# Optimization experiments

Measured on AMD Instinct MI355X. Metric: run time of the kernel, lower is better.

The kernel has to match this reference:

```python
import jax
import jax.numpy as jnp
from jax import lax
import numpy as np

B, C, H, W = 16, 96, 112, 112
HIDDEN = 4 * C
LN_EPS = 1e-6  # ConvNeXt LayerNorm eps


def setup_inputs() -> dict:
    key = jax.random.key(0)
    ks = jax.random.split(key, 8)
    x = jax.random.normal(ks[0], (B, C, H, W), dtype=jnp.float32)
    # depthwise 7x7 kernel, HWIO with feature_group_count=C -> (7,7,1,C)
    dw_w = jax.random.normal(ks[1], (7, 7, 1, C), dtype=jnp.float32) * 0.02
    dw_b = jnp.zeros((C,), dtype=jnp.float32)
    gamma = jnp.ones((C,), dtype=jnp.float32)
    beta = jnp.zeros((C,), dtype=jnp.float32)
    w1 = jax.random.normal(ks[2], (C, HIDDEN), dtype=jnp.float32) * 0.02
    b1 = jnp.zeros((HIDDEN,), dtype=jnp.float32)
    w2 = jax.random.normal(ks[3], (HIDDEN, C), dtype=jnp.float32) * 0.02
    b2 = jnp.zeros((C,), dtype=jnp.float32)
    scale = jnp.full((C,), 1e-6, dtype=jnp.float32)  # block_scale init 1e-6
    return {"x": x, "dw_w": dw_w, "dw_b": dw_b, "gamma": gamma, "beta": beta,
            "w1": w1, "b1": b1, "w2": w2, "b2": b2, "scale": scale}


def reference(x, dw_w, dw_b, gamma, beta, w1, b1, w2, b2, scale):
    # depthwise 7x7, stride 1, padding 3 (SAME), groups = C
    y = lax.conv_general_dilated(
        x, dw_w, window_strides=(1, 1), padding="SAME",
        dimension_numbers=("NCHW", "HWIO", "NCHW"),
        feature_group_count=C,
    ) + dw_b[None, :, None, None]
    # BCHW -> BHWC
    y = jnp.transpose(y, (0, 2, 3, 1))
    # LayerNorm over channel dim
    mu = jnp.mean(y, axis=-1, keepdims=True)
    var = jnp.var(y, axis=-1, keepdims=True)
    y = (y - mu) * lax.rsqrt(var + LN_EPS) * gamma + beta
    # pointwise MLP with exact GELU (torch nn.GELU default)
    h = jax.nn.gelu(jnp.einsum("bhwc,cd->bhwd", y, w1) + b1, approximate=False)
    y = jnp.einsum("bhwd,dc->bhwc", h, w2) + b2
    # BHWC -> BCHW, scale, residual (eval mode: stochastic depth = identity)
    y = jnp.transpose(y, (0, 3, 1, 2))
    return scale[None, :, None, None] * y + x
```

## Files before the change

### kernel.cpp

```cpp
#include <hip/hip_runtime.h>
#include <hip/hip_bf16.h>

#define BATCH 16
#define CCH 96
#define HH 112
#define WW 112
#define HID 384
#define NPIX (BATCH * HH * WW)
#define HW (HH * WW)

#define PXB 128
#define ZROWD 50
#define HSLICE 6144
#define RING_SLOTS 6
#define ZR_BYTES (PXB * ZROWD * 4)
#define B1_OFF (RING_SLOTS * HSLICE)
#define SMEM_TOTAL (B1_OFF + 1536)

typedef __attribute__((ext_vector_type(8))) short bf16x8;
typedef __attribute__((ext_vector_type(4))) float f32x4;
typedef __attribute__((ext_vector_type(4))) unsigned int uint4v;

typedef const __attribute__((address_space(1))) void gvoid_t;
typedef __attribute__((address_space(3))) void svoid_t;

__device__ __forceinline__ short f2bf(float v) {
    __hip_bfloat16 h = __float2bfloat16(v);
    return __builtin_bit_cast(short, h);
}
__device__ __forceinline__ float bf2f(short s) {
    unsigned int u = ((unsigned int)(unsigned short)s) << 16;
    return __builtin_bit_cast(float, u);
}
__device__ __forceinline__ float gelu_fast(float v) {
    float e = __expf(-1.702f * v);
    return v * __builtin_amdgcn_rcpf(1.0f + e);
}

__global__ __launch_bounds__(256) void pack_w(const float* __restrict__ w1,
                                              const float* __restrict__ w2,
                                              const float* __restrict__ gamma,
                                              const float* __restrict__ scale,
                                              short* __restrict__ wp) {
    int o = blockIdx.x * 256 + threadIdx.x;
    if (o >= 12 * 12 * 64 * 8) return;
    const int j   = o & 7;
    const int l   = (o >> 3) & 63;
    const int g   = o >> 9;
    const int f   = g % 12;
    const int kk2 = g / 12;
    float v;
    if (f < 6) {
        const int kk = f >> 1, mh = f & 1;
        const int c  = kk * 32 + (l >> 4) * 8 + j;
        const int d  = (2 * kk2 + mh) * 16 + (l & 15);
        v = gamma[c] * w1[c * HID + d];
    } else {
        const int nt2 = f - 6;
        const int dd  = kk2 * 32 + ((j >> 2) << 4) + ((l >> 4) << 2) + (j & 3);
        const int n   = nt2 * 16 + (l & 15);
        v = w2[dd * CCH + n] * scale[n];
    }
    wp[o] = f2bf(v);
}

__global__ __launch_bounds__(256) void pack_bias(const float* __restrict__ w1,
                                                 const float* __restrict__ b1,
                                                 const float* __restrict__ beta,
                                                 const float* __restrict__ b2,
                                                 const float* __restrict__ scale,
                                                 float* __restrict__ b1p,
                                                 float* __restrict__ b2p) {
    int t = blockIdx.x * 256 + threadIdx.x;
    if (t < HID) {
        float s = b1[t];
        for (int c = 0; c < CCH; ++c) s += beta[c] * w1[c * HID + t];
        b1p[t] = s;
    } else if (t < HID + CCH) {
        int c = t - HID;
        b2p[c] = scale[c] * b2[c];
    }
}

__global__ __launch_bounds__(256) void conv_kernel(
    const float* __restrict__ x, const float* __restrict__ dww,
    const float* __restrict__ dwb, short* __restrict__ y)
{
    __shared__ float xs[34][128];

    const int t = threadIdx.x;
    const int p = blockIdx.x;
    int o = (p & 7) * 768 + (p >> 3);
    const int ht = o & 3;  o >>= 2;
    const int c  = o % CCH;
    const int b  = o / CCH;
    const int h0 = ht * 28;
    const float* xc = x + (size_t)(b * CCH + c) * HW;

    float4 vbuf[5];
    #pragma unroll
    for (int k = 0; k < 5; ++k) {
        const int idx = t + 256 * k;
        const int r  = idx >> 5;
        const int j  = idx & 31;
        const int gh = h0 - 3 + r;
        float4 v = make_float4(0.f, 0.f, 0.f, 0.f);
        if (idx < 1088 && (unsigned)gh < HH && j >= 1 && j <= 28)
            v = *reinterpret_cast<const float4*>(xc + gh * WW + 4 * j - 4);
        vbuf[k] = v;
    }
    #pragma unroll
    for (int k = 0; k < 5; ++k) {
        const int idx = t + 256 * k;
        if (idx < 1088)
            *reinterpret_cast<float4*>(&xs[0][0] + (idx >> 5) * 128 + (idx & 31) * 4) = vbuf[k];
    }
    __syncthreads();

    const int col = t & 127;
    const int rg  = t >> 7;
    if (col < WW) {
        const int r0 = rg * 14;
        const float bias = dwb[c];
        float acc[14];
        #pragma unroll
        for (int r = 0; r < 14; ++r) acc[r] = bias;
        #pragma unroll
        for (int kw = 0; kw < 7; ++kw) {
            float cv[20];
            #pragma unroll
            for (int i = 0; i < 20; ++i) cv[i] = xs[r0 + i][col + kw + 1];
            #pragma unroll
            for (int kh = 0; kh < 7; ++kh) {
                const float wt = dww[(kh * 7 + kw) * CCH + c];
                #pragma unroll
                for (int r = 0; r < 14; ++r) acc[r] += cv[r + kh] * wt;
            }
        }
        short* yc = y + (size_t)(b * CCH + c) * HW + (h0 + r0) * WW + col;
        #pragma unroll
        for (int r = 0; r < 14; ++r) yc[r * WW] = f2bf(acc[r]);
    }
}

__global__ __launch_bounds__(256, 4) void mlp_kernel(
    const short* __restrict__ ybuf, const char* __restrict__ wp,
    const float* __restrict__ b1p, const float* __restrict__ b2p,
    const float* __restrict__ x, float* __restrict__ out)
{
    __shared__ __align__(16) char smem[SMEM_TOTAL];
    unsigned int* zr = (unsigned int*)smem;
    float* b1l = (float*)(smem + B1_OFF);

    const int t    = threadIdx.x;
    const int lane = t & 63;
    const int wv   = t >> 6;
    const int l15  = lane & 15;
    const int q    = lane >> 4;
    const int px0  = blockIdx.x * PXB;
    const int b    = px0 / HW;
    const int hw0  = px0 - b * HW;
    const int c0 = (wv < 2) ? 2 * wv : wv + 2;
    const int c1 = (wv < 2) ? 2 * wv + 1 : wv + 2;

    if (t < 192) {
        const int pq = t / 48;
        const int cp = t - pq * 48;
        const unsigned int* Ap = (const unsigned int*)(ybuf +
            (size_t)(b * CCH + 2 * cp) * HW + hw0 + pq * 32);
        const unsigned int* Bp = (const unsigned int*)(ybuf +
            (size_t)(b * CCH + 2 * cp + 1) * HW + hw0 + pq * 32);
        #pragma unroll
        for (int e = 0; e < 4; ++e) {
            const uint4v A  = *reinterpret_cast<const uint4v*>(Ap + e * 4);
            const uint4v Bv = *reinterpret_cast<const uint4v*>(Bp + e * 4);
            #pragma unroll
            for (int k = 0; k < 4; ++k) {
                const int px = pq * 32 + e * 8 + 2 * k;
                zr[px * ZROWD + cp]       = (A[k] & 0xffffu) | (Bv[k] << 16);
                zr[(px + 1) * ZROWD + cp] = (A[k] >> 16) | (Bv[k] & 0xffff0000u);
            }
        }
    } else {
        const int i0 = (t - 192) * 6;
        #pragma unroll
        for (int i2 = 0; i2 < 6; ++i2) b1l[i0 + i2] = b1p[i0 + i2];
    }

    f32x4 acc2[2][6];
    #pragma unroll
    for (int nt2 = 0; nt2 < 6; ++nt2) {
        const int c = nt2 * 16 + l15;
        const float bv = b2p[c];
        #pragma unroll
        for (int m2 = 0; m2 < 2; ++m2) {
            const size_t g = (size_t)(b * CCH + c) * HW + hw0 + wv * 32 + m2 * 16 + q * 4;
            const f32x4 xv = *reinterpret_cast<const f32x4*>(x + g);
            acc2[m2][nt2].x = bv + xv.x;  acc2[m2][nt2].y = bv + xv.y;
            acc2[m2][nt2].z = bv + xv.z;  acc2[m2][nt2].w = bv + xv.w;
        }
    }
    __syncthreads();

    bf16x8 za[2][3];
    #pragma unroll
    for (int nt = 0; nt < 2; ++nt) {
        const int row = wv * 32 + nt * 16 + l15;
        const char* base = smem + row * (ZROWD * 4) + q * 16;
        float s1 = 0.f, s2 = 0.f;
        #pragma unroll
        for (int kk = 0; kk < 3; ++kk) {
            za[nt][kk] = *reinterpret_cast<const bf16x8*>(base + kk * 64);
            #pragma unroll
            for (int j = 0; j < 8; ++j) {
                const float v = bf2f(za[nt][kk][j]);
                s1 += v; s2 += v * v;
            }
        }
        s1 += __shfl_xor(s1, 16, 64);  s2 += __shfl_xor(s2, 16, 64);
        s1 += __shfl_xor(s1, 32, 64);  s2 += __shfl_xor(s2, 32, 64);
        const float mu   = s1 * (1.0f / CCH);
        const float rstd = rsqrtf(s2 * (1.0f / CCH) - mu * mu + 1e-6f);
        #pragma unroll
        for (int kk = 0; kk < 3; ++kk)
            #pragma unroll
            for (int j = 0; j < 8; ++j)
                za[nt][kk][j] = f2bf((bf2f(za[nt][kk][j]) - mu) * rstd);
    }
    __syncthreads();

    asm volatile("s_waitcnt vmcnt(0)" ::: "memory");

    #define STAGE_H(HS, SLOT)                                                       \
        {                                                                           \
            const char* _s = wp + (size_t)(HS) * HSLICE + lane * 16;                \
            char* _d = smem + (SLOT) * HSLICE;                                      \
            __builtin_amdgcn_global_load_lds((gvoid_t*)(_s + c0 * 1024),            \
                                             (svoid_t*)(_d + c0 * 1024), 16, 0, 0); \
            __builtin_amdgcn_global_load_lds((gvoid_t*)(_s + c1 * 1024),            \
                                             (svoid_t*)(_d + c1 * 1024), 16, 0, 0); \
        }
    #define WAITBAR()                                                               \
        {                                                                           \
            asm volatile("s_waitcnt vmcnt(8)" ::: "memory");                        \
            __builtin_amdgcn_s_barrier();                                           \
            __builtin_amdgcn_sched_barrier(0);                                      \
        }

    STAGE_H(0, 0);
    STAGE_H(1, 1);
    STAGE_H(2, 2);
    STAGE_H(3, 3);

    #pragma unroll
    for (int kk2 = 0; kk2 < 12; ++kk2) {
        {
            const int hs = (2 * kk2 + 4 > 23) ? 23 : 2 * kk2 + 4;
            STAGE_H(hs, hs % RING_SLOTS);
        }
        WAITBAR();
        const char* wb1 = smem + ((2 * kk2) % RING_SLOTS) * HSLICE + lane * 16;

        f32x4 p0[2], p1[2];
        const f32x4 bva = *reinterpret_cast<const f32x4*>(b1l + 32 * kk2 + q * 4);
        const f32x4 bvb = *reinterpret_cast<const f32x4*>(b1l + 32 * kk2 + 16 + q * 4);
        p0[0] = bva;  p0[1] = bva;
        p1[0] = bvb;  p1[1] = bvb;
        #pragma unroll
        for (int kk = 0; kk < 3; ++kk) {
            const bf16x8 wfa = *reinterpret_cast<const bf16x8*>(wb1 + (kk * 2) * 1024);
            const bf16x8 wfb = *reinterpret_cast<const bf16x8*>(wb1 + (kk * 2 + 1) * 1024);
            p0[0] = __builtin_amdgcn_mfma_f32_16x16x32_bf16(wfa, za[0][kk], p0[0], 0, 0, 0);
            p0[1] = __builtin_amdgcn_mfma_f32_16x16x32_bf16(wfa, za[1][kk], p0[1], 0, 0, 0);
            p1[0] = __builtin_amdgcn_mfma_f32_16x16x32_bf16(wfb, za[0][kk], p1[0], 0, 0, 0);
            p1[1] = __builtin_amdgcn_mfma_f32_16x16x32_bf16(wfb, za[1][kk], p1[1], 0, 0, 0);
        }
        bf16x8 hv[2];
        #pragma unroll
        for (int nt = 0; nt < 2; ++nt)
            #pragma unroll
            for (int i = 0; i < 4; ++i) {
                hv[nt][i]     = f2bf(gelu_fast(p0[nt][i]));
                hv[nt][4 + i] = f2bf(gelu_fast(p1[nt][i]));
            }

        {
            const int hs = (2 * kk2 + 5 > 23) ? 23 : 2 * kk2 + 5;
            STAGE_H(hs, hs % RING_SLOTS);
        }
        WAITBAR();
        const char* wb2 = smem + ((2 * kk2 + 1) % RING_SLOTS) * HSLICE + lane * 16;
        #pragma unroll
        for (int nt2 = 0; nt2 < 6; ++nt2) {
            const bf16x8 bfr = *reinterpret_cast<const bf16x8*>(wb2 + nt2 * 1024);
            acc2[0][nt2] = __builtin_amdgcn_mfma_f32_16x16x32_bf16(hv[0], bfr, acc2[0][nt2], 0, 0, 0);
            acc2[1][nt2] = __builtin_amdgcn_mfma_f32_16x16x32_bf16(hv[1], bfr, acc2[1][nt2], 0, 0, 0);
        }
    }
    #undef STAGE_H
    #undef WAITBAR

    #pragma unroll
    for (int m2 = 0; m2 < 2; ++m2) {
        const int pxl = hw0 + wv * 32 + m2 * 16 + q * 4;
        #pragma unroll
        for (int nt2 = 0; nt2 < 6; ++nt2) {
            const int c = nt2 * 16 + l15;
            const size_t g = (size_t)(b * CCH + c) * HW + pxl;
            *reinterpret_cast<f32x4*>(out + g) = acc2[m2][nt2];
        }
    }
}

extern "C" void kernel_launch(void* const* d_in, const int* in_sizes, int n_in,
                              void* d_out, int out_size, void* d_ws, size_t ws_size,
                              hipStream_t stream) {
    const float* x     = (const float*)d_in[0];
    const float* dww   = (const float*)d_in[1];
    const float* dwb   = (const float*)d_in[2];
    const float* gamma = (const float*)d_in[3];
    const float* beta  = (const float*)d_in[4];
    const float* w1    = (const float*)d_in[5];
    const float* b1    = (const float*)d_in[6];
    const float* w2    = (const float*)d_in[7];
    const float* b2    = (const float*)d_in[8];
    const float* scale = (const float*)d_in[9];
    float* out = (float*)d_out;

    char* ws = (char*)d_ws;
    short* ybuf = (short*)ws;
    const size_t Y_BYTES = (size_t)NPIX * CCH * 2;
    short* wp  = (short*)(ws + Y_BYTES);
    float* b1p = (float*)(ws + Y_BYTES + 24 * HSLICE);
    float* b2p = b1p + HID;

    pack_w<<<(12 * 12 * 64 * 8 + 255) / 256, 256, 0, stream>>>(w1, w2, gamma, scale, wp);
    pack_bias<<<2, 256, 0, stream>>>(w1, b1, beta, b2, scale, b1p, b2p);
    conv_kernel<<<BATCH * CCH * 4, 256, 0, stream>>>(x, dww, dwb, ybuf);
    mlp_kernel<<<NPIX / PXB, 256, 0, stream>>>(ybuf, (const char*)wp, b1p, b2p, x, out);
}
```

Before: 121.7 us.

## Merge W1/W2 weight slices into one staged chunk per iteration and pack conv FMAs

The MLP weight staging ring now moves one combined 12KB slice (W1 and W2 parts together) per outer iteration, with 3 ring slots and lookahead of one slice. This halves the barriers per iteration, from two to one. Each wave now issues three global-to-LDS loads instead of two. Separately, the depthwise conv accumulates pairs of rows in float2 vectors so the compiler can emit packed FMA instructions. The trade-off is less prefetch depth (1 slice ahead instead of 4 half-slices), which may expose load latency, and shared memory per block stays the same.

```diff
diff --git a/kernel.cpp b/kernel.cpp
--- a/kernel.cpp
+++ b/kernel.cpp
@@ -11,14 +11,15 @@
 
 #define PXB 128
 #define ZROWD 50
-#define HSLICE 6144
-#define RING_SLOTS 6
+#define SLICE_B 12288
+#define RING_SLOTS 3
 #define ZR_BYTES (PXB * ZROWD * 4)
-#define B1_OFF (RING_SLOTS * HSLICE)
+#define B1_OFF (RING_SLOTS * SLICE_B)
 #define SMEM_TOTAL (B1_OFF + 1536)
 
 typedef __attribute__((ext_vector_type(8))) short bf16x8;
 typedef __attribute__((ext_vector_type(4))) float f32x4;
+typedef __attribute__((ext_vector_type(2))) float f32x2;
 typedef __attribute__((ext_vector_type(4))) unsigned int uint4v;
 
 typedef const __attribute__((address_space(1))) void gvoid_t;
@@ -122,9 +123,9 @@
     if (col < WW) {
         const int r0 = rg * 14;
         const float bias = dwb[c];
-        float acc[14];
-        #pragma unroll
-        for (int r = 0; r < 14; ++r) acc[r] = bias;
+        f32x2 accp[7];
+        #pragma unroll
+        for (int r = 0; r < 7; ++r) accp[r] = (f32x2){bias, bias};
         #pragma unroll
         for (int kw = 0; kw < 7; ++kw) {
             float cv[20];
@@ -133,13 +134,22 @@
             #pragma unroll
             for (int kh = 0; kh < 7; ++kh) {
                 const float wt = dww[(kh * 7 + kw) * CCH + c];
+                const f32x2 wt2 = (f32x2){wt, wt};
                 #pragma unroll
-                for (int r = 0; r < 14; ++r) acc[r] += cv[r + kh] * wt;
+                for (int r = 0; r < 7; ++r) {
+                    f32x2 v;
+                    v.x = cv[2 * r + kh];
+                    v.y = cv[2 * r + kh + 1];
+                    accp[r] += v * wt2;
+                }
             }
         }
         short* yc = y + (size_t)(b * CCH + c) * HW + (h0 + r0) * WW + col;
         #pragma unroll
-        for (int r = 0; r < 14; ++r) yc[r * WW] = f2bf(acc[r]);
+        for (int r = 0; r < 7; ++r) {
+            yc[(2 * r) * WW]     = f2bf(accp[r].x);
+            yc[(2 * r + 1) * WW] = f2bf(accp[r].y);
+        }
     }
 }
 
@@ -160,8 +170,6 @@
     const int px0  = blockIdx.x * PXB;
     const int b    = px0 / HW;
     const int hw0  = px0 - b * HW;
-    const int c0 = (wv < 2) ? 2 * wv : wv + 2;
-    const int c1 = (wv < 2) ? 2 * wv + 1 : wv + 2;
 
     if (t < 192) {
         const int pq = t / 48;
@@ -231,35 +239,32 @@
 
     asm volatile("s_waitcnt vmcnt(0)" ::: "memory");
 
-    #define STAGE_H(HS, SLOT)                                                       \
+    #define STAGE_F(SL, SLOT)                                                       \
         {                                                                           \
-            const char* _s = wp + (size_t)(HS) * HSLICE + lane * 16;                \
-            char* _d = smem + (SLOT) * HSLICE;                                      \
-            __builtin_amdgcn_global_load_lds((gvoid_t*)(_s + c0 * 1024),            \
-                                             (svoid_t*)(_d + c0 * 1024), 16, 0, 0); \
-            __builtin_amdgcn_global_load_lds((gvoid_t*)(_s + c1 * 1024),            \
-                                             (svoid_t*)(_d + c1 * 1024), 16, 0, 0); \
+            const char* _s = wp + (size_t)(SL) * SLICE_B + (wv * 3) * 1024 +        \
+                             lane * 16;                                             \
+            char* _d = smem + (SLOT) * SLICE_B + (wv * 3) * 1024;                   \
+            __builtin_amdgcn_global_load_lds((gvoid_t*)(_s),        (svoid_t*)(_d),        16, 0, 0); \
+            __builtin_amdgcn_global_load_lds((gvoid_t*)(_s + 1024), (svoid_t*)(_d + 1024), 16, 0, 0); \
+            __builtin_amdgcn_global_load_lds((gvoid_t*)(_s + 2048), (svoid_t*)(_d + 2048), 16, 0, 0); \
         }
     #define WAITBAR()                                                               \
         {                                                                           \
-            asm volatile("s_waitcnt vmcnt(8)" ::: "memory");                        \
+            asm volatile("s_waitcnt vmcnt(3)" ::: "memory");                        \
             __builtin_amdgcn_s_barrier();                                           \
             __builtin_amdgcn_sched_barrier(0);                                      \
         }
 
-    STAGE_H(0, 0);
-    STAGE_H(1, 1);
-    STAGE_H(2, 2);
-    STAGE_H(3, 3);
+    STAGE_F(0, 0);
 
     #pragma unroll
     for (int kk2 = 0; kk2 < 12; ++kk2) {
         {
-            const int hs = (2 * kk2 + 4 > 23) ? 23 : 2 * kk2 + 4;
-            STAGE_H(hs, hs % RING_SLOTS);
+            const int sl = (kk2 + 1 > 11) ? 11 : kk2 + 1;
+            STAGE_F(sl, sl % RING_SLOTS);
         }
         WAITBAR();
-        const char* wb1 = smem + ((2 * kk2) % RING_SLOTS) * HSLICE + lane * 16;
+        const char* wb = smem + (kk2 % RING_SLOTS) * SLICE_B + lane * 16;
 
         f32x4 p0[2], p1[2];
         const f32x4 bva = *reinterpret_cast<const f32x4*>(b1l + 32 * kk2 + q * 4);
@@ -268,8 +273,8 @@
         p1[0] = bvb;  p1[1] = bvb;
         #pragma unroll
         for (int kk = 0; kk < 3; ++kk) {
-            const bf16x8 wfa = *reinterpret_cast<const bf16x8*>(wb1 + (kk * 2) * 1024);
-            const bf16x8 wfb = *reinterpret_cast<const bf16x8*>(wb1 + (kk * 2 + 1) * 1024);
+            const bf16x8 wfa = *reinterpret_cast<const bf16x8*>(wb + (kk * 2) * 1024);
+            const bf16x8 wfb = *reinterpret_cast<const bf16x8*>(wb + (kk * 2 + 1) * 1024);
             p0[0] = __builtin_amdgcn_mfma_f32_16x16x32_bf16(wfa, za[0][kk], p0[0], 0, 0, 0);
             p0[1] = __builtin_amdgcn_mfma_f32_16x16x32_bf16(wfa, za[1][kk], p0[1], 0, 0, 0);
             p1[0] = __builtin_amdgcn_mfma_f32_16x16x32_bf16(wfb, za[0][kk], p1[0], 0, 0, 0);
@@ -283,21 +288,14 @@
                 hv[nt][i]     = f2bf(gelu_fast(p0[nt][i]));
                 hv[nt][4 + i] = f2bf(gelu_fast(p1[nt][i]));
             }
-
-        {
-            const int hs = (2 * kk2 + 5 > 23) ? 23 : 2 * kk2 + 5;
-            STAGE_H(hs, hs % RING_SLOTS);
-        }
-        WAITBAR();
-        const char* wb2 = smem + ((2 * kk2 + 1) % RING_SLOTS) * HSLICE + lane * 16;
         #pragma unroll
         for (int nt2 = 0; nt2 < 6; ++nt2) {
-            const bf16x8 bfr = *reinterpret_cast<const bf16x8*>(wb2 + nt2 * 1024);
+            const bf16x8 bfr = *reinterpret_cast<const bf16x8*>(wb + (6 + nt2) * 1024);
             acc2[0][nt2] = __builtin_amdgcn_mfma_f32_16x16x32_bf16(hv[0], bfr, acc2[0][nt2], 0, 0, 0);
             acc2[1][nt2] = __builtin_amdgcn_mfma_f32_16x16x32_bf16(hv[1], bfr, acc2[1][nt2], 0, 0, 0);
         }
     }
-    #undef STAGE_H
+    #undef STAGE_F
     #undef WAITBAR
 
     #pragma unroll
@@ -331,7 +329,7 @@
     short* ybuf = (short*)ws;
     const size_t Y_BYTES = (size_t)NPIX * CCH * 2;
     short* wp  = (short*)(ws + Y_BYTES);
-    float* b1p = (float*)(ws + Y_BYTES + 24 * HSLICE);
+    float* b1p = (float*)(ws + Y_BYTES + 12 * SLICE_B);
     float* b2p = b1p + HID;
 
     pack_w<<<(12 * 12 * 64 * 8 + 255) / 256, 256, 0, stream>>>(w1, w2, gamma, scale, wp);
```

Result: faster. 116.2 us (-4.5%).
